# Performance work log

Hardware: AMD Instinct MI355X
Metric: run time of the kernel (lower is better)

Reference implementation:

```python
import jax, jax.numpy as jnp
import numpy as np

B, T, D, MP = 32, 256, 512, 20


def setup_inputs() -> dict:
    key = jax.random.key(0)
    k1, k2, k3 = jax.random.split(key, 3)
    reps_lt = jax.random.normal(k1, (B, T, D), dtype=jnp.float32)
    reps_rt = jax.random.normal(k2, (B, T, D), dtype=jnp.float32)
    kernel = jax.random.normal(k3, (1, 1, 1, MP, D), dtype=jnp.float32)
    return {"reps_lt": reps_lt, "reps_rt": reps_rt, "kernel": kernel}


def reference(reps_lt, reps_rt, kernel):
    # kernel: (1,1,1,m,d) -> (m,d)
    km = kernel.reshape(kernel.shape[-2], kernel.shape[-1])
    # scores[b,t,s,m] = sum_d lt[b,t,d] * km[m,d] * rt[b,s,d]
    # matches original broadcast-multiply + sum over d (cosine_norm=False path)
    scores = jnp.einsum('btd,md,bsd->btsm', reps_lt, km, reps_rt)
    match = jnp.tanh(scores)               # [b, t1, t2, m]
    return jnp.max(match, axis=2)          # max-pool over t2 -> [b, t1, m]
```

## Files before the change

### kernel.cpp

```cpp
#include <hip/hip_runtime.h>


constexpr int TT = 256;
constexpr int DD = 512;
constexpr int NM = 20;
constexpr int NB = 32;
constexpr int BM = 64;

typedef float f32x4 __attribute__((ext_vector_type(4)));
typedef int   i32x8 __attribute__((ext_vector_type(8)));

__device__ __forceinline__ unsigned pack_bf16(float lo, float hi) {
    unsigned ulo = __builtin_bit_cast(unsigned, lo);
    unsigned uhi = __builtin_bit_cast(unsigned, hi);
    return (ulo >> 16) | (uhi & 0xFFFF0000u);
}

__device__ __forceinline__ unsigned pk4_fp8(float a, float b, float c, float d) {
    unsigned r = __builtin_amdgcn_cvt_pk_fp8_f32(a, b, 0, false);
    return __builtin_amdgcn_cvt_pk_fp8_f32(c, d, r, true);
}

__device__ __forceinline__ float blo(unsigned u) { return __builtin_bit_cast(float, u << 16); }
__device__ __forceinline__ float bhi(unsigned u) { return __builtin_bit_cast(float, u); }

__device__ __forceinline__ i32x8 mk8(uint4 a, uint4 b) {
    i32x8 v;
    v[0] = (int)a.x; v[1] = (int)a.y; v[2] = (int)a.z; v[3] = (int)a.w;
    v[4] = (int)b.x; v[5] = (int)b.y; v[6] = (int)b.z; v[7] = (int)b.w;
    return v;
}

__device__ __forceinline__ void gld_lds16(const void* g, void* l) {
    __builtin_amdgcn_global_load_lds(
        (const __attribute__((address_space(1))) void*)g,
        (__attribute__((address_space(3))) void*)l, 16, 0, 0);
}

__global__ __launch_bounds__(256)
void cast_inputs(const float* __restrict__ lt, const float* __restrict__ rt,
                 unsigned short* __restrict__ ltb, unsigned char* __restrict__ rtf)
{
    const int bid = (int)blockIdx.x;
    if (bid < 2048) {
        size_t base = ((size_t)bid * 256 + threadIdx.x) * 8;
        float4 a = *(const float4*)(lt + base);
        float4 b = *(const float4*)(lt + base + 4);
        uint4 w;
        w.x = pack_bf16(a.x, a.y);
        w.y = pack_bf16(a.z, a.w);
        w.z = pack_bf16(b.x, b.y);
        w.w = pack_bf16(b.z, b.w);
        *(uint4*)(ltb + base) = w;
    } else {
        const unsigned o = (unsigned)(bid - 2048) * 256 + threadIdx.x;
        const int lane = o & 63;
        const int h    = (o >> 6) & 1;
        const int g    = (o >> 7) & 15;
        const int kk   = (o >> 11) & 3;
        const int b    = o >> 13;
        const int s    = g * 16 + (lane & 15);
        const int d0   = kk * 128 + (lane >> 4) * 32 + h * 16;
        const float* p = rt + ((size_t)b * TT + s) * DD + d0;
        float4 x0 = *(const float4*)p;
        float4 x1 = *(const float4*)(p + 4);
        float4 x2 = *(const float4*)(p + 8);
        float4 x3 = *(const float4*)(p + 12);
        uint4 w;
        w.x = pk4_fp8(x0.x, x0.y, x0.z, x0.w);
        w.y = pk4_fp8(x1.x, x1.y, x1.z, x1.w);
        w.z = pk4_fp8(x2.x, x2.y, x2.z, x2.w);
        w.w = pk4_fp8(x3.x, x3.y, x3.z, x3.w);
        *(uint4*)(rtf + (size_t)o * 16) = w;
    }
}

__global__ __launch_bounds__(256, 3)
void mp_match_mx(const unsigned short* __restrict__ ltb, const unsigned char* __restrict__ rtf,
                 const float* __restrict__ km, float* __restrict__ out)
{
    __shared__ __attribute__((aligned(16))) uint4 Ash[BM * 33];
    __shared__ __attribute__((aligned(16))) unsigned char Bsh[2][8192];
    __shared__ __attribute__((aligned(16))) float maxbuf[4][BM];

    const int f  = blockIdx.x;
    const int c8 = f & 7;
    const int i  = f >> 3;
    const int b  = c8 + 8 * (i / 80);
    const int j  = i % 80;
    const int m  = j >> 2;
    const int t0 = (j & 3) * BM;

    const int tid  = threadIdx.x;
    const int w    = tid >> 6;
    const int lane = tid & 63;
    const int l15  = lane & 15;
    const int l4   = lane >> 4;

    const unsigned short* ltB = ltb + ((size_t)b * TT + t0) * DD;
    const unsigned char*  rtT = rtf + (size_t)b * (TT * DD);
    const float*          kmp = km  + (size_t)m * DD;

    auto stageB = [&](int u) {
        const int kk = u >> 2, q = u & 3;
        const unsigned char* g = rtT + kk * 32768 + (q * 4 + w) * 2048 + lane * 16;
        unsigned char* l = &Bsh[u & 1][w * 2048];
        gld_lds16(g, l);
        gld_lds16(g + 1024, l + 1024);
    };

    stageB(0);

    const int cc = tid & 31, r0 = (tid >> 5) * 8;
    const float4 kA = *(const float4*)(kmp + cc * 16);
    const float4 kB = *(const float4*)(kmp + cc * 16 + 4);
    const float4 kC = *(const float4*)(kmp + cc * 16 + 8);
    const float4 kD = *(const float4*)(kmp + cc * 16 + 12);
#pragma unroll
    for (int r = 0; r < 8; ++r) {
        const unsigned short* src = ltB + (size_t)(r0 + r) * DD + cc * 16;
        uint4 h0 = *(const uint4*)src;
        uint4 h1 = *(const uint4*)(src + 8);
        uint4 o;
        o.x = pk4_fp8(blo(h0.x) * kA.x, bhi(h0.x) * kA.y, blo(h0.y) * kA.z, bhi(h0.y) * kA.w);
        o.y = pk4_fp8(blo(h0.z) * kB.x, bhi(h0.z) * kB.y, blo(h0.w) * kB.z, bhi(h0.w) * kB.w);
        o.z = pk4_fp8(blo(h1.x) * kC.x, bhi(h1.x) * kC.y, blo(h1.y) * kC.z, bhi(h1.y) * kC.w);
        o.w = pk4_fp8(blo(h1.z) * kD.x, bhi(h1.z) * kD.y, blo(h1.w) * kD.z, bhi(h1.w) * kD.w);
        Ash[(r0 + r) * 33 + cc] = o;
    }
    __syncthreads();

    f32x4 acc[4][4] = {};
    i32x8 av[4];

#pragma unroll
    for (int u = 0; u < 16; ++u) {
        const int kk = u >> 2, q = u & 3;
        if (u + 1 < 16) {
            stageB(u + 1);
            asm volatile("s_waitcnt vmcnt(2)" ::: "memory");
        } else {
            asm volatile("s_waitcnt vmcnt(0)" ::: "memory");
        }
        if (q == 0) {
#pragma unroll
            for (int ii = 0; ii < 4; ++ii) {
                const int base = (ii * 16 + l15) * 33 + kk * 8 + l4 * 2;
                av[ii] = mk8(Ash[base], Ash[base + 1]);
            }
        }
        const uint4* bp = (const uint4*)&Bsh[u & 1][w * 2048];
        i32x8 bv = mk8(bp[lane], bp[64 + lane]);
#pragma unroll
        for (int ii = 0; ii < 4; ++ii)
            acc[ii][q] = __builtin_amdgcn_mfma_scale_f32_16x16x128_f8f6f4(
                av[ii], bv, acc[ii][q], 0, 0, 0, 127, 0, 127);
    }

#pragma unroll
    for (int ii = 0; ii < 4; ++ii) {
        f32x4 v = acc[ii][0];
#pragma unroll
        for (int q = 1; q < 4; ++q) {
            v.x = fmaxf(v.x, acc[ii][q].x);
            v.y = fmaxf(v.y, acc[ii][q].y);
            v.z = fmaxf(v.z, acc[ii][q].z);
            v.w = fmaxf(v.w, acc[ii][q].w);
        }
#pragma unroll
        for (int off = 1; off < 16; off <<= 1) {
            v.x = fmaxf(v.x, __shfl_xor(v.x, off, 64));
            v.y = fmaxf(v.y, __shfl_xor(v.y, off, 64));
            v.z = fmaxf(v.z, __shfl_xor(v.z, off, 64));
            v.w = fmaxf(v.w, __shfl_xor(v.w, off, 64));
        }
        if (l15 == 0)
            *(f32x4*)&maxbuf[w][ii * 16 + l4 * 4] = v;
    }
    __syncthreads();
    if (tid < BM) {
        float v = fmaxf(fmaxf(maxbuf[0][tid], maxbuf[1][tid]),
                        fmaxf(maxbuf[2][tid], maxbuf[3][tid]));
        out[((size_t)b * TT + t0 + tid) * NM + m] = tanhf(v);
    }
}

typedef short bf16x8 __attribute__((ext_vector_type(8)));

__global__ __launch_bounds__(256, 2)
void mp_match_kernel(const float* __restrict__ lt, const float* __restrict__ rt,
                     const float* __restrict__ km, float* __restrict__ out)
{
    __shared__ __attribute__((aligned(16))) unsigned short Ash[2][4][128][8];
    __shared__ __attribute__((aligned(16))) unsigned short Bsh2[2][4][256][8];
    __shared__ __attribute__((aligned(16))) float maxbuf[2][128];

    const int ttile = blockIdx.x, m = blockIdx.y, b = blockIdx.z;
    const int t0 = ttile * 128;
    const int tid = threadIdx.x, wave = tid >> 6, lane = tid & 63;
    const int l15 = lane & 15, l4 = lane >> 4;
    const int wt = (wave & 1) * 64, wsi = wave >> 1;

    const float* ltp = lt + ((size_t)b * TT + t0) * DD;
    const float* rtp = rt + (size_t)b * TT * DD;
    const float* kmp = km + (size_t)m * DD;
    const int a_t = tid >> 1, a_h = tid & 1;

    f32x4 acc[4][8] = {};

    auto stage = [&](int kk, int buf) {
        const int d0 = kk * 32;
        const float* ap = ltp + (size_t)a_t * DD + d0 + a_h * 16;
        const float* kp = kmp + d0 + a_h * 16;
#pragma unroll
        for (int q = 0; q < 2; ++q) {
            float4 x0 = *(const float4*)(ap + q * 8);
            float4 x1 = *(const float4*)(ap + q * 8 + 4);
            float4 k0 = *(const float4*)(kp + q * 8);
            float4 k1 = *(const float4*)(kp + q * 8 + 4);
            uint4 wv;
            wv.x = pack_bf16(x0.x * k0.x, x0.y * k0.y);
            wv.y = pack_bf16(x0.z * k0.z, x0.w * k0.w);
            wv.z = pack_bf16(x1.x * k1.x, x1.y * k1.y);
            wv.w = pack_bf16(x1.z * k1.z, x1.w * k1.w);
            *(uint4*)&Ash[buf][a_h * 2 + q][a_t][0] = wv;
        }
        const float* bp = rtp + (size_t)tid * DD + d0;
#pragma unroll
        for (int p = 0; p < 4; ++p) {
            float4 y0 = *(const float4*)(bp + p * 8);
            float4 y1 = *(const float4*)(bp + p * 8 + 4);
            uint4 wv;
            wv.x = pack_bf16(y0.x, y0.y);
            wv.y = pack_bf16(y0.z, y0.w);
            wv.z = pack_bf16(y1.x, y1.y);
            wv.w = pack_bf16(y1.z, y1.w);
            *(uint4*)&Bsh2[buf][p][tid][0] = wv;
        }
    };

    stage(0, 0);
    for (int kk = 0; kk < 16; ++kk) {
        const int buf = kk & 1;
        __syncthreads();
        bf16x8 af[4], bfv[8];
#pragma unroll
        for (int i2 = 0; i2 < 4; ++i2)
            af[i2] = *(const bf16x8*)&Ash[buf][l4][wt + i2 * 16 + l15][0];
#pragma unroll
        for (int j2 = 0; j2 < 8; ++j2)
            bfv[j2] = *(const bf16x8*)&Bsh2[buf][l4][wsi * 128 + j2 * 16 + l15][0];
        if (kk + 1 < 16) stage(kk + 1, buf ^ 1);
#pragma unroll
        for (int i2 = 0; i2 < 4; ++i2)
#pragma unroll
            for (int j2 = 0; j2 < 8; ++j2)
                acc[i2][j2] = __builtin_amdgcn_mfma_f32_16x16x32_bf16(af[i2], bfv[j2], acc[i2][j2], 0, 0, 0);
    }
#pragma unroll
    for (int i2 = 0; i2 < 4; ++i2) {
        f32x4 v = acc[i2][0];
#pragma unroll
        for (int j2 = 1; j2 < 8; ++j2) {
            v.x = fmaxf(v.x, acc[i2][j2].x); v.y = fmaxf(v.y, acc[i2][j2].y);
            v.z = fmaxf(v.z, acc[i2][j2].z); v.w = fmaxf(v.w, acc[i2][j2].w);
        }
#pragma unroll
        for (int off = 1; off < 16; off <<= 1) {
            v.x = fmaxf(v.x, __shfl_xor(v.x, off, 64));
            v.y = fmaxf(v.y, __shfl_xor(v.y, off, 64));
            v.z = fmaxf(v.z, __shfl_xor(v.z, off, 64));
            v.w = fmaxf(v.w, __shfl_xor(v.w, off, 64));
        }
        if (l15 == 0) *(f32x4*)&maxbuf[wsi][wt + i2 * 16 + l4 * 4] = v;
    }
    __syncthreads();
    if (tid < 128) {
        float v = fmaxf(maxbuf[0][tid], maxbuf[1][tid]);
        out[((size_t)b * TT + t0 + tid) * NM + m] = tanhf(v);
    }
}

extern "C" void kernel_launch(void* const* d_in, const int* in_sizes, int n_in,
                              void* d_out, int out_size, void* d_ws, size_t ws_size,
                              hipStream_t stream) {
    const float* lt  = (const float*)d_in[0];
    const float* rt  = (const float*)d_in[1];
    const float* km  = (const float*)d_in[2];
    float*       out = (float*)d_out;

    const size_t elems = (size_t)NB * TT * DD;
    const size_t ltbB  = elems * sizeof(unsigned short);
    const size_t rtfB  = elems;

    if (ws_size >= ltbB + rtfB) {
        unsigned short* ltb = (unsigned short*)d_ws;
        unsigned char*  rtf = (unsigned char*)((char*)d_ws + ltbB);
        cast_inputs<<<3072, 256, 0, stream>>>(lt, rt, ltb, rtf);
        mp_match_mx<<<2560, 256, 0, stream>>>(ltb, rtf, km, out);
    } else {
        mp_match_kernel<<<dim3(2, NM, NB), 256, 0, stream>>>(lt, rt, km, out);
    }
}
```

Measured before the change: 116.5 us.

## Drop bf16 lt pre-cast and stream fp8 rt tiles through register ring

Removes the bf16 staging of reps_lt, so the pre-cast kernel now converts only reps_rt to fp8 and the match kernel reads fp32 lt directly, applying the km scale and fp8 conversion itself. The B operand is no longer staged into LDS with global_load_lds and manual waitcnt. Each wave now loads its fp8 fragments straight into a 4-deep register ring, prefetched three steps ahead. This saves a cast pass, workspace traffic and LDS use, at the cost of twice the lt bytes per block (read repeatedly across 20 m-blocks) and extra registers at the 3-blocks-per-CU launch bound.

Result: faster. 110.4 us (-5.3%).

```diff
diff --git a/kernel.cpp b/kernel.cpp
--- a/kernel.cpp
+++ b/kernel.cpp
@@ -21,9 +21,6 @@
     return __builtin_amdgcn_cvt_pk_fp8_f32(c, d, r, true);
 }
 
-__device__ __forceinline__ float blo(unsigned u) { return __builtin_bit_cast(float, u << 16); }
-__device__ __forceinline__ float bhi(unsigned u) { return __builtin_bit_cast(float, u); }
-
 __device__ __forceinline__ i32x8 mk8(uint4 a, uint4 b) {
     i32x8 v;
     v[0] = (int)a.x; v[1] = (int)a.y; v[2] = (int)a.z; v[3] = (int)a.w;
@@ -31,56 +28,35 @@
     return v;
 }
 
-__device__ __forceinline__ void gld_lds16(const void* g, void* l) {
-    __builtin_amdgcn_global_load_lds(
-        (const __attribute__((address_space(1))) void*)g,
-        (__attribute__((address_space(3))) void*)l, 16, 0, 0);
-}
-
 __global__ __launch_bounds__(256)
-void cast_inputs(const float* __restrict__ lt, const float* __restrict__ rt,
-                 unsigned short* __restrict__ ltb, unsigned char* __restrict__ rtf)
+void cast_rt(const float* __restrict__ rt, unsigned char* __restrict__ rtf)
 {
-    const int bid = (int)blockIdx.x;
-    if (bid < 2048) {
-        size_t base = ((size_t)bid * 256 + threadIdx.x) * 8;
-        float4 a = *(const float4*)(lt + base);
-        float4 b = *(const float4*)(lt + base + 4);
-        uint4 w;
-        w.x = pack_bf16(a.x, a.y);
-        w.y = pack_bf16(a.z, a.w);
-        w.z = pack_bf16(b.x, b.y);
-        w.w = pack_bf16(b.z, b.w);
-        *(uint4*)(ltb + base) = w;
-    } else {
-        const unsigned o = (unsigned)(bid - 2048) * 256 + threadIdx.x;
-        const int lane = o & 63;
-        const int h    = (o >> 6) & 1;
-        const int g    = (o >> 7) & 15;
-        const int kk   = (o >> 11) & 3;
-        const int b    = o >> 13;
-        const int s    = g * 16 + (lane & 15);
-        const int d0   = kk * 128 + (lane >> 4) * 32 + h * 16;
-        const float* p = rt + ((size_t)b * TT + s) * DD + d0;
-        float4 x0 = *(const float4*)p;
-        float4 x1 = *(const float4*)(p + 4);
-        float4 x2 = *(const float4*)(p + 8);
-        float4 x3 = *(const float4*)(p + 12);
-        uint4 w;
-        w.x = pk4_fp8(x0.x, x0.y, x0.z, x0.w);
-        w.y = pk4_fp8(x1.x, x1.y, x1.z, x1.w);
-        w.z = pk4_fp8(x2.x, x2.y, x2.z, x2.w);
-        w.w = pk4_fp8(x3.x, x3.y, x3.z, x3.w);
-        *(uint4*)(rtf + (size_t)o * 16) = w;
-    }
+    const unsigned o = (unsigned)blockIdx.x * 256 + threadIdx.x;
+    const int lane = o & 63;
+    const int h    = (o >> 6) & 1;
+    const int g    = (o >> 7) & 15;
+    const int kk   = (o >> 11) & 3;
+    const int b    = o >> 13;
+    const int s    = g * 16 + (lane & 15);
+    const int d0   = kk * 128 + (lane >> 4) * 32 + h * 16;
+    const float* p = rt + ((size_t)b * TT + s) * DD + d0;
+    float4 x0 = *(const float4*)p;
+    float4 x1 = *(const float4*)(p + 4);
+    float4 x2 = *(const float4*)(p + 8);
+    float4 x3 = *(const float4*)(p + 12);
+    uint4 w;
+    w.x = pk4_fp8(x0.x, x0.y, x0.z, x0.w);
+    w.y = pk4_fp8(x1.x, x1.y, x1.z, x1.w);
+    w.z = pk4_fp8(x2.x, x2.y, x2.z, x2.w);
+    w.w = pk4_fp8(x3.x, x3.y, x3.z, x3.w);
+    *(uint4*)(rtf + (size_t)o * 16) = w;
 }
 
 __global__ __launch_bounds__(256, 3)
-void mp_match_mx(const unsigned short* __restrict__ ltb, const unsigned char* __restrict__ rtf,
+void mp_match_mx(const float* __restrict__ lt, const unsigned char* __restrict__ rtf,
                  const float* __restrict__ km, float* __restrict__ out)
 {
     __shared__ __attribute__((aligned(16))) uint4 Ash[BM * 33];
-    __shared__ __attribute__((aligned(16))) unsigned char Bsh[2][8192];
     __shared__ __attribute__((aligned(16))) float maxbuf[4][BM];
 
     const int f  = blockIdx.x;
@@ -97,19 +73,18 @@
     const int l15  = lane & 15;
     const int l4   = lane >> 4;
 
-    const unsigned short* ltB = ltb + ((size_t)b * TT + t0) * DD;
-    const unsigned char*  rtT = rtf + (size_t)b * (TT * DD);
-    const float*          kmp = km  + (size_t)m * DD;
-
-    auto stageB = [&](int u) {
-        const int kk = u >> 2, q = u & 3;
-        const unsigned char* g = rtT + kk * 32768 + (q * 4 + w) * 2048 + lane * 16;
-        unsigned char* l = &Bsh[u & 1][w * 2048];
-        gld_lds16(g, l);
-        gld_lds16(g + 1024, l + 1024);
+    const float*         ltB  = lt  + ((size_t)b * TT + t0) * DD;
+    const float*         kmp  = km  + (size_t)m * DD;
+    const unsigned char* rtB0 = rtf + (size_t)b * (TT * DD) + w * 2048 + lane * 16;
+
+    uint4 ring[4][2];
+    auto loadB = [&](int u) {
+        const unsigned char* p = rtB0 + u * 8192;
+        ring[u & 3][0] = *(const uint4*)p;
+        ring[u & 3][1] = *(const uint4*)(p + 1024);
     };
 
-    stageB(0);
+    loadB(0); loadB(1); loadB(2);
 
     const int cc = tid & 31, r0 = (tid >> 5) * 8;
     const float4 kA = *(const float4*)(kmp + cc * 16);
@@ -118,14 +93,16 @@
     const float4 kD = *(const float4*)(kmp + cc * 16 + 12);
 #pragma unroll
     for (int r = 0; r < 8; ++r) {
-        const unsigned short* src = ltB + (size_t)(r0 + r) * DD + cc * 16;
-        uint4 h0 = *(const uint4*)src;
-        uint4 h1 = *(const uint4*)(src + 8);
+        const float* src = ltB + (size_t)(r0 + r) * DD + cc * 16;
+        float4 x0 = *(const float4*)src;
+        float4 x1 = *(const float4*)(src + 4);
+        float4 x2 = *(const float4*)(src + 8);
+        float4 x3 = *(const float4*)(src + 12);
         uint4 o;
-        o.x = pk4_fp8(blo(h0.x) * kA.x, bhi(h0.x) * kA.y, blo(h0.y) * kA.z, bhi(h0.y) * kA.w);
-        o.y = pk4_fp8(blo(h0.z) * kB.x, bhi(h0.z) * kB.y, blo(h0.w) * kB.z, bhi(h0.w) * kB.w);
-        o.z = pk4_fp8(blo(h1.x) * kC.x, bhi(h1.x) * kC.y, blo(h1.y) * kC.z, bhi(h1.y) * kC.w);
-        o.w = pk4_fp8(blo(h1.z) * kD.x, bhi(h1.z) * kD.y, blo(h1.w) * kD.z, bhi(h1.w) * kD.w);
+        o.x = pk4_fp8(x0.x * kA.x, x0.y * kA.y, x0.z * kA.z, x0.w * kA.w);
+        o.y = pk4_fp8(x1.x * kB.x, x1.y * kB.y, x1.z * kB.z, x1.w * kB.w);
+        o.z = pk4_fp8(x2.x * kC.x, x2.y * kC.y, x2.z * kC.z, x2.w * kC.w);
+        o.w = pk4_fp8(x3.x * kD.x, x3.y * kD.y, x3.z * kD.z, x3.w * kD.w);
         Ash[(r0 + r) * 33 + cc] = o;
     }
     __syncthreads();
@@ -136,12 +113,7 @@
 #pragma unroll
     for (int u = 0; u < 16; ++u) {
         const int kk = u >> 2, q = u & 3;
-        if (u + 1 < 16) {
-            stageB(u + 1);
-            asm volatile("s_waitcnt vmcnt(2)" ::: "memory");
-        } else {
-            asm volatile("s_waitcnt vmcnt(0)" ::: "memory");
-        }
+        if (u + 3 < 16) loadB(u + 3);
         if (q == 0) {
 #pragma unroll
             for (int ii = 0; ii < 4; ++ii) {
@@ -149,8 +121,7 @@
                 av[ii] = mk8(Ash[base], Ash[base + 1]);
             }
         }
-        const uint4* bp = (const uint4*)&Bsh[u & 1][w * 2048];
-        i32x8 bv = mk8(bp[lane], bp[64 + lane]);
+        i32x8 bv = mk8(ring[u & 3][0], ring[u & 3][1]);
 #pragma unroll
         for (int ii = 0; ii < 4; ++ii)
             acc[ii][q] = __builtin_amdgcn_mfma_scale_f32_16x16x128_f8f6f4(
@@ -290,14 +261,12 @@
     float*       out = (float*)d_out;
 
     const size_t elems = (size_t)NB * TT * DD;
-    const size_t ltbB  = elems * sizeof(unsigned short);
     const size_t rtfB  = elems;
 
-    if (ws_size >= ltbB + rtfB) {
-        unsigned short* ltb = (unsigned short*)d_ws;
-        unsigned char*  rtf = (unsigned char*)((char*)d_ws + ltbB);
-        cast_inputs<<<3072, 256, 0, stream>>>(lt, rt, ltb, rtf);
-        mp_match_mx<<<2560, 256, 0, stream>>>(ltb, rtf, km, out);
+    if (ws_size >= rtfB) {
+        unsigned char* rtf = (unsigned char*)d_ws;
+        cast_rt<<<1024, 256, 0, stream>>>(rt, rtf);
+        mp_match_mx<<<2560, 256, 0, stream>>>(lt, rtf, km, out);
     } else {
         mp_match_kernel<<<dim3(2, NM, NB), 256, 0, stream>>>(lt, rt, km, out);
     }
```
